# Performance work log

Hardware: AMD Instinct MI355X
Metric: run time of the kernel (lower is better)

Reference implementation:

```python
import jax, jax.numpy as jnp
import numpy as np

EPS = 1e-5

def binarize(x):
    # sign binarization with straight-through estimator (matches .data replacement in torch BNN code)
    s = jnp.where(x >= 0, 1.0, -1.0).astype(x.dtype)
    return x + jax.lax.stop_gradient(s - x)

def conv3x3(x, w):
    return jax.lax.conv_general_dilated(x, w, (1, 1), ((1, 1), (1, 1)),
                                        dimension_numbers=('NCHW', 'OIHW', 'NCHW'))

def bn4(x, g, b, m, v):
    inv = jax.lax.rsqrt(v + EPS)
    return (x - m[None, :, None, None]) * (g * inv)[None, :, None, None] + b[None, :, None, None]

def bn2(x, g, b, m, v):
    return (x - m) * (g * jax.lax.rsqrt(v + EPS)) + b

def maxpool2(x):
    return jax.lax.reduce_window(x, -jnp.inf, jax.lax.max, (1, 1, 2, 2), (1, 1, 2, 2), 'VALID')

def ht(x):
    return jnp.clip(x, -1.0, 1.0)


def setup_inputs() -> dict:
    key = jax.random.key(0)
    ks = iter(jax.random.split(key, 64))
    d = {}
    d['x'] = jax.random.normal(next(ks), (256, 3, 32, 32), jnp.float32)
    conv_shapes = [(128, 3), (128, 128), (256, 128), (256, 256), (512, 256), (512, 512)]
    for i, (co, ci) in enumerate(conv_shapes, start=1):
        d[f'w{i}'] = jax.random.normal(next(ks), (co, ci, 3, 3), jnp.float32) * 0.05
        d[f'g{i}'] = jax.random.uniform(next(ks), (co,), jnp.float32, 0.5, 1.5)
        d[f'b{i}'] = jax.random.normal(next(ks), (co,), jnp.float32) * 0.1
        d[f'm{i}'] = jax.random.normal(next(ks), (co,), jnp.float32) * 0.1
        d[f'v{i}'] = jax.random.uniform(next(ks), (co,), jnp.float32, 0.5, 1.5)
    d['bias2'] = jax.random.normal(next(ks), (128,), jnp.float32) * 0.1  # conv2 has default bias=True
    fc_shapes = [(1024, 512 * 4 * 4), (1024, 1024), (10, 1024)]
    for j, (co, ci) in enumerate(fc_shapes, start=7):
        d[f'w{j}'] = jax.random.normal(next(ks), (co, ci), jnp.float32) * 0.02
        d[f'm{j}'] = jax.random.normal(next(ks), (co,), jnp.float32) * 0.1
        d[f'v{j}'] = jax.random.uniform(next(ks), (co,), jnp.float32, 0.5, 1.5)
        if j < 9:  # last BN is affine=False
            d[f'g{j}'] = jax.random.uniform(next(ks), (co,), jnp.float32, 0.5, 1.5)
            d[f'b{j}'] = jax.random.normal(next(ks), (co,), jnp.float32) * 0.1
    return d


def reference(x, w1, g1, b1, m1, v1, w2, bias2, g2, b2, m2, v2, w3, g3, b3, m3, v3,
              w4, g4, b4, m4, v4, w5, g5, b5, m5, v5, w6, g6, b6, m6, v6,
              w7, g7, b7, m7, v7, w8, g8, b8, m8, v8, w9, m9, v9):
    # features
    h = conv3x3(x, binarize(w1))                      # first layer: input NOT binarized (3 channels)
    h = ht(bn4(h, g1, b1, m1, v1))
    h = conv3x3(binarize(h), binarize(w2)) + bias2[None, :, None, None]
    h = ht(bn4(maxpool2(h), g2, b2, m2, v2))
    h = conv3x3(binarize(h), binarize(w3))
    h = ht(bn4(h, g3, b3, m3, v3))
    h = conv3x3(binarize(h), binarize(w4))
    h = ht(bn4(maxpool2(h), g4, b4, m4, v4))
    h = conv3x3(binarize(h), binarize(w5))
    h = ht(bn4(h, g5, b5, m5, v5))
    h = conv3x3(binarize(h), binarize(w6))
    h = ht(bn4(maxpool2(h), g6, b6, m6, v6))          # [B, 512, 4, 4]
    # classifier
    h = h.reshape(-1, 512 * 4 * 4)
    h = ht(bn2(binarize(h) @ binarize(w7).T, g7, b7, m7, v7))
    h = ht(bn2(binarize(h) @ binarize(w8).T, g8, b8, m8, v8))
    h = binarize(h) @ binarize(w9).T
    h = (h - m9) * jax.lax.rsqrt(v9 + EPS)            # BatchNorm1d(affine=False)
    return jax.nn.log_softmax(h, axis=-1)
```

## Files before the change

kernel.cpp:

```cpp
#include <hip/hip_runtime.h>
#include <stdint.h>

typedef unsigned long long u64;

static __device__ __forceinline__ int uread(int v) { return __builtin_amdgcn_readfirstlane(v); }
static __device__ __forceinline__ float fr(float x) { __asm__ volatile("" : "+v"(x)); return x; }

static __device__ __forceinline__ float bn_scale(float g, float v) {
    return fr(g * fr(1.0f / fr(sqrtf(fr(v + 1e-5f)))));
}
static __device__ __forceinline__ bool bn_neg_s(float x, float si, float b, float m) {
    float t1 = fr(x - m);
    float t2 = fr(t1 * si);
    float bn = fr(t2 + b);
    return bn < 0.0f;
}


__device__ __forceinline__ void d_packw1(const float* __restrict__ w, float* __restrict__ ws, int id) {
    if (id >= 27 * 128) return;
    int co = id & 127, j = id >> 7;
    ws[j * 128 + co] = (w[co * 27 + j] < 0.f) ? -1.f : 1.f;
}

__device__ __forceinline__ void d_pack_conv(const float* __restrict__ w, u64* __restrict__ wb,
                                            int CINW, int COUT, int wv, int lane) {
    int wrd = wv % CINW, co = wv / CINW;
    int CIN = CINW * 64;
    const float* p = w + ((size_t)co * CIN + (size_t)wrd * 64 + lane) * 9;
    float f[9];
#pragma unroll
    for (int t = 0; t < 9; ++t) f[t] = p[t];
#pragma unroll
    for (int t = 0; t < 9; ++t) {
        u64 bits = __ballot(f[t] < 0.f);
        if (lane == 0) wb[(size_t)(t * CINW + wrd) * COUT + co] = bits;
    }
}

__device__ __forceinline__ void d_packw7(const float* __restrict__ w, u64* __restrict__ wb, int wv, int lane) {
    int cw = wv & 7, o = wv >> 3;
    const float* p = w + (size_t)o * 8192 + (size_t)(cw * 64 + lane) * 16;
    float f[16];
#pragma unroll
    for (int i = 0; i < 16; i += 4) {
        float4 q = *(const float4*)(p + i);
        f[i] = q.x; f[i + 1] = q.y; f[i + 2] = q.z; f[i + 3] = q.w;
    }
#pragma unroll
    for (int pixel = 0; pixel < 16; ++pixel) {
        u64 bits = __ballot(f[pixel] < 0.f);
        if (lane == 0) wb[(size_t)(pixel * 8 + cw) * 1024 + o] = bits;
    }
}

__device__ __forceinline__ void d_packw8(const float* __restrict__ w, u64* __restrict__ wb, int wv, int lane) {
    int k = wv & 15, o = wv >> 4;
    float f = w[(size_t)o * 1024 + k * 64 + lane];
    u64 bits = __ballot(f < 0.f);
    if (lane == 0) wb[(size_t)k * 1024 + o] = bits;
}

__device__ __forceinline__ void d_packw9(const float* __restrict__ w, u64* __restrict__ wb, int wv, int lane) {
    if (wv >= 160) return;
    int k = wv & 15, o = wv >> 4;
    float f = w[(size_t)o * 1024 + k * 64 + lane];
    u64 bits = __ballot(f < 0.f);
    if (lane == 0) wb[k * 16 + o] = bits;
}

__global__ __launch_bounds__(256) void pack_all_kernel(
    const float* __restrict__ w1, float* __restrict__ w1s,
    const float* __restrict__ w2, u64* __restrict__ w2p,
    const float* __restrict__ w3, u64* __restrict__ w3p,
    const float* __restrict__ w4, u64* __restrict__ w4p,
    const float* __restrict__ w5, u64* __restrict__ w5p,
    const float* __restrict__ w6, u64* __restrict__ w6p,
    const float* __restrict__ w7, u64* __restrict__ w7p,
    const float* __restrict__ w8, u64* __restrict__ w8p,
    const float* __restrict__ w9, u64* __restrict__ w9p)
{
    int b = blockIdx.x;
    int lane = threadIdx.x & 63;
    int wq = threadIdx.x >> 6;
    if (b < 14) { d_packw1(w1, w1s, b * 256 + threadIdx.x); return; } b -= 14;
    if (b < 64) { d_pack_conv(w2, w2p, 2, 128, b * 4 + wq, lane); return; } b -= 64;
    if (b < 128) { d_pack_conv(w3, w3p, 2, 256, b * 4 + wq, lane); return; } b -= 128;
    if (b < 256) { d_pack_conv(w4, w4p, 4, 256, b * 4 + wq, lane); return; } b -= 256;
    if (b < 512) { d_pack_conv(w5, w5p, 4, 512, b * 4 + wq, lane); return; } b -= 512;
    if (b < 1024) { d_pack_conv(w6, w6p, 8, 512, b * 4 + wq, lane); return; } b -= 1024;
    if (b < 2048) { d_packw7(w7, w7p, b * 4 + wq, lane); return; } b -= 2048;
    if (b < 4096) { d_packw8(w8, w8p, b * 4 + wq, lane); return; } b -= 4096;
    d_packw9(w9, w9p, b * 4 + wq, lane);
}

__global__ __launch_bounds__(256, 4) void conv1_kernel(
    const float* __restrict__ x, const float* __restrict__ w1s,
    const float* __restrict__ g, const float* __restrict__ bb,
    const float* __restrict__ m, const float* __restrict__ v,
    u64* __restrict__ out, int N)
{
    int lane = threadIdx.x & 63;
    int rid = uread(blockIdx.x * 4 + (threadIdx.x >> 6));
    if (rid >= N * 32) return;
    int n = rid >> 5, y = rid & 31;
    const float* xb = x + (size_t)n * 3072;
    const bool rv0 = (y > 0), rv2 = (y < 31);
    const int y0 = rv0 ? y - 1 : 0, y2 = rv2 ? y + 1 : 31;

    int co0 = lane, co1 = 64 + lane;
    float w0[27], w1[27];
#pragma unroll
    for (int j = 0; j < 27; ++j) {
        w0[j] = fr(w1s[j * 128 + co0]);
        w1[j] = fr(w1s[j * 128 + co1]);
    }
    float b0 = bb[co0], m0 = m[co0];
    float b1 = bb[co1], m1 = m[co1];
    float si0 = bn_scale(g[co0], v[co0]);
    float si1 = bn_scale(g[co1], v[co1]);

    float cm[9], cc[9], cn[9];
#pragma unroll
    for (int t = 0; t < 9; ++t) cm[t] = 0.f;

    auto ldcol = [&](float* c, int xs) {
#pragma unroll
        for (int ci = 0; ci < 3; ++ci) {
            float a0 = xb[ci * 1024 + y0 * 32 + xs];
            float a1 = xb[ci * 1024 + y  * 32 + xs];
            float a2 = xb[ci * 1024 + y2 * 32 + xs];
            c[0 + ci] = fr(rv0 ? a0 : 0.f);
            c[3 + ci] = fr(a1);
            c[6 + ci] = fr(rv2 ? a2 : 0.f);
        }
    };
    ldcol(cc, 0);

    u64* orow = out + (((size_t)n * 32 + y) * 32) * 2;

    for (int xx = 0; xx < 32; ++xx) {
        if (xx < 31) ldcol(cn, xx + 1);
        else {
#pragma unroll
            for (int t = 0; t < 9; ++t) cn[t] = 0.f;
        }
        float a0 = 0.f, a1 = 0.f;
#pragma unroll
        for (int ky = 0; ky < 3; ++ky) {
#pragma unroll
            for (int ci = 0; ci < 3; ++ci) a0 = fmaf(w0[ci * 9 + ky * 3 + 0], cm[ky * 3 + ci], a0);
#pragma unroll
            for (int ci = 0; ci < 3; ++ci) a0 = fmaf(w0[ci * 9 + ky * 3 + 1], cc[ky * 3 + ci], a0);
#pragma unroll
            for (int ci = 0; ci < 3; ++ci) a0 = fmaf(w0[ci * 9 + ky * 3 + 2], cn[ky * 3 + ci], a0);
        }
#pragma unroll
        for (int ky = 0; ky < 3; ++ky) {
#pragma unroll
            for (int ci = 0; ci < 3; ++ci) a1 = fmaf(w1[ci * 9 + ky * 3 + 0], cm[ky * 3 + ci], a1);
#pragma unroll
            for (int ci = 0; ci < 3; ++ci) a1 = fmaf(w1[ci * 9 + ky * 3 + 1], cc[ky * 3 + ci], a1);
#pragma unroll
            for (int ci = 0; ci < 3; ++ci) a1 = fmaf(w1[ci * 9 + ky * 3 + 2], cn[ky * 3 + ci], a1);
        }
        u64 bits0 = __ballot(bn_neg_s(a0, si0, b0, m0));
        u64 bits1 = __ballot(bn_neg_s(a1, si1, b1, m1));
        if (lane == 0) {
            ulonglong2 st; st.x = bits0; st.y = bits1;
            *(ulonglong2*)(orow + xx * 2) = st;
        }
#pragma unroll
        for (int t = 0; t < 9; ++t) { cm[t] = cc[t]; cc[t] = cn[t]; }
    }
}

template<int WORDS, int COW, bool POOL, bool HAS_BIAS, int H, int YS, int NWAVES, int MINW>
__global__ __launch_bounds__(NWAVES * 64, MINW) void binconv_lds(
    const u64* __restrict__ a, const u64* __restrict__ wb,
    const float* __restrict__ g, const float* __restrict__ bb,
    const float* __restrict__ m, const float* __restrict__ v,
    const float* __restrict__ bias, u64* __restrict__ out, int N)
{
    const int W = H;
    const int OH = POOL ? H / 2 : H, OW = POOL ? W / 2 : W;
    const int COUT = COW * 64;
    const int OROWS = OH / YS;
    const int RMAX = POOL ? OROWS * 2 + 2 : OROWS + 2;
    const int PR = POOL ? 4 : 3;
    const int NW = POOL ? 4 : 1;
    const int W2 = WORDS / 2;
    const int S = POOL ? 2 : 1;
    const int NBC = 9 * WORDS * 64;
    const int GPX = (OW <= 4) ? OW : ((NW == 4) ? 4 : OW);
    const int NG = OW / GPX;

    __shared__ alignas(16) u64 tile[RMAX * W * WORDS];

    int blk = blockIdx.x;
    int ys = blk % YS, n = blk / YS;
    int oy0 = ys * OROWS;
    int iy0 = (POOL ? oy0 * 2 - 1 : oy0 - 1); if (iy0 < 0) iy0 = 0;
    int iy1 = (POOL ? (oy0 + OROWS - 1) * 2 + 2 : oy0 + OROWS); if (iy1 > H - 1) iy1 = H - 1;
    int R = iy1 - iy0 + 1;
    {
        const u64* src = a + ((size_t)(n * H + iy0) * W) * WORDS;
        int tot = R * W * WORDS;
        for (int i = threadIdx.x; i < tot; i += NWAVES * 64) tile[i] = src[i];
    }
    __syncthreads();

    int lane = threadIdx.x & 63;
    int wv = uread((int)(threadIdx.x >> 6));

    int cw0, r0, r1;
    if (COW >= NWAVES) { cw0 = wv; r0 = 0; r1 = OROWS; }
    else { cw0 = wv % COW; int chunk = OROWS * COW / NWAVES; r0 = (wv / COW) * chunk; r1 = r0 + chunk; }

    const ulonglong2* t2 = (const ulonglong2*)tile;

    for (int cw = cw0; cw < COW; cw += NWAVES) {
        int co = cw * 64 + lane;
        float bc = bb[co], mc = m[co];
        float sic = bn_scale(g[co], v[co]);
        float bi = HAS_BIAS ? bias[co] : 0.f;

        auto store_px = [&](int oy, int ox, int best) {
            float tv = (float)best;
            if (HAS_BIAS) tv = fr(tv + bi);
            u64 bits = __ballot(bn_neg_s(tv, sic, bc, mc));
            if (lane == 0) out[((size_t)(n * OH + oy) * OW + ox) * COW + cw] = bits;
        };

        if constexpr (W2 == 1) {
            u64 wgt[18];
#pragma unroll
            for (int t = 0; t < 18; ++t) wgt[t] = wb[(size_t)t * COUT + co];

            auto px_general = [&](int oy, int ox) {
                int y0 = (POOL ? oy * 2 : oy) - 1;
                bool rv[PR];
#pragma unroll
                for (int p = 0; p < PR; ++p) rv[p] = ((unsigned)(y0 + p) < (unsigned)H);
                int x0 = (POOL ? ox * 2 : ox) - 1;
                bool cv[PR];
#pragma unroll
                for (int q = 0; q < PR; ++q) cv[q] = ((unsigned)(x0 + q) < (unsigned)W);

                int acc[NW], nb[NW];
#pragma unroll
                for (int i = 0; i < NW; ++i) { acc[i] = 0; nb[i] = 0; }
#pragma unroll
                for (int sy = 0; sy < (POOL ? 2 : 1); ++sy)
#pragma unroll
                for (int sx = 0; sx < (POOL ? 2 : 1); ++sx)
#pragma unroll
                for (int ky = 0; ky < 3; ++ky)
#pragma unroll
                for (int kx = 0; kx < 3; ++kx)
                    if (rv[sy + ky] && cv[sx + kx]) nb[POOL ? sy * 2 + sx : 0] += WORDS * 64;

                ulonglong2 pt[PR][PR];
#pragma unroll
                for (int p = 0; p < PR; ++p) if (rv[p]) {
                    int lrow = y0 + p - iy0;
#pragma unroll
                    for (int q = 0; q < PR; ++q) if (cv[q])
                        pt[p][q] = t2[(lrow * W + (x0 + q))];
                }
#pragma unroll
                for (int sy = 0; sy < (POOL ? 2 : 1); ++sy)
#pragma unroll
                for (int sx = 0; sx < (POOL ? 2 : 1); ++sx)
#pragma unroll
                for (int ky = 0; ky < 3; ++ky)
#pragma unroll
                for (int kx = 0; kx < 3; ++kx)
                    if (rv[sy + ky] && cv[sx + kx]) {
                        ulonglong2 q = pt[sy + ky][sx + kx];
                        int wi = POOL ? sy * 2 + sx : 0;
                        acc[wi] += __popcll(q.x ^ wgt[(ky * 3 + kx) * 2])
                                 + __popcll(q.y ^ wgt[(ky * 3 + kx) * 2 + 1]);
                    }
                int best = 0;
#pragma unroll
                for (int i = 0; i < NW; ++i) {
                    int dot = nb[i] - 2 * acc[i];
                    best = (i == 0) ? dot : max(best, dot);
                }
                store_px(oy, ox, best);
            };

            for (int oy = oy0 + r0; oy < oy0 + r1; ++oy) {
                int y0 = (POOL ? oy * 2 : oy) - 1;
                if (y0 < 0 || y0 + PR > H) {
                    for (int ox = 0; ox < OW; ++ox) px_general(oy, ox);
                    continue;
                }
                int base = y0 - iy0;
                px_general(oy, 0);
                {
                    ulonglong2 win[PR][PR];
                    const int xl = POOL ? 1 : 0;
#pragma unroll
                    for (int p = 0; p < PR; ++p)
#pragma unroll
                        for (int q = 0; q < PR; ++q)
                            win[p][q] = t2[(base + p) * W + xl + q];
#pragma unroll
                    for (int ox = 1; ox < OW - 1; ++ox) {
                        int acc[NW];
#pragma unroll
                        for (int i = 0; i < NW; ++i) acc[i] = 0;
#pragma unroll
                        for (int sy = 0; sy < (POOL ? 2 : 1); ++sy)
#pragma unroll
                        for (int sx = 0; sx < (POOL ? 2 : 1); ++sx)
#pragma unroll
                        for (int ky = 0; ky < 3; ++ky)
#pragma unroll
                        for (int kx = 0; kx < 3; ++kx) {
                            ulonglong2 q = win[sy + ky][sx + kx];
                            int wi = POOL ? sy * 2 + sx : 0;
                            acc[wi] += __popcll(q.x ^ wgt[(ky * 3 + kx) * 2])
                                     + __popcll(q.y ^ wgt[(ky * 3 + kx) * 2 + 1]);
                        }
                        int best = 0;
#pragma unroll
                        for (int i = 0; i < NW; ++i) {
                            int dot = NBC - 2 * acc[i];
                            best = (i == 0) ? dot : max(best, dot);
                        }
                        store_px(oy, ox, best);
                        if (ox < OW - 2) {
                            const int xnew = S * ox - 1 + PR;
#pragma unroll
                            for (int p = 0; p < PR; ++p) {
#pragma unroll
                                for (int q = 0; q < PR - S; ++q) win[p][q] = win[p][q + S];
#pragma unroll
                                for (int s = 0; s < S; ++s)
                                    win[p][PR - S + s] = t2[(base + p) * W + xnew + s];
                            }
                        }
                    }
                }
                px_general(oy, OW - 1);
            }
        } else {
            for (int oy = oy0 + r0; oy < oy0 + r1; ++oy) {
                int y0r = (POOL ? oy * 2 : oy) - 1;
                bool rv[PR];
#pragma unroll
                for (int p = 0; p < PR; ++p) rv[p] = ((unsigned)(y0r + p) < (unsigned)H);
                int baseR = y0r - iy0;

#pragma unroll
                for (int gg = 0; gg < NG; ++gg) {
                    int acc[GPX][NW];
#pragma unroll
                    for (int i = 0; i < GPX; ++i)
#pragma unroll
                        for (int wi = 0; wi < NW; ++wi) acc[i][wi] = 0;

#pragma unroll 1
                    for (int w2 = 0; w2 < W2; ++w2) {
                        u64 wc[18];
#pragma unroll
                        for (int t = 0; t < 9; ++t) {
                            wc[t * 2]     = wb[(size_t)(t * WORDS + 2 * w2) * COUT + co];
                            wc[t * 2 + 1] = wb[(size_t)(t * WORDS + 2 * w2 + 1) * COUT + co];
                        }
#pragma unroll
                        for (int i = 0; i < GPX; ++i) {
                            const int ox = gg * GPX + i;
                            const int x0 = S * ox - 1;
                            ulonglong2 pt[PR][PR];
#pragma unroll
                            for (int p = 0; p < PR; ++p) {
                                if (rv[p]) {
#pragma unroll
                                    for (int q = 0; q < PR; ++q) {
                                        const int x = x0 + q;
                                        if (x >= 0 && x < W)
                                            pt[p][q] = t2[((baseR + p) * W + x) * W2 + w2];
                                    }
                                }
                            }
#pragma unroll
                            for (int sy = 0; sy < (POOL ? 2 : 1); ++sy)
#pragma unroll
                            for (int sx = 0; sx < (POOL ? 2 : 1); ++sx)
#pragma unroll
                            for (int ky = 0; ky < 3; ++ky)
#pragma unroll
                            for (int kx = 0; kx < 3; ++kx) {
                                const int xq = x0 + sx + kx;
                                if (xq >= 0 && xq < W) {
                                    if (rv[sy + ky]) {
                                        ulonglong2 q = pt[sy + ky][sx + kx];
                                        const int t = ky * 3 + kx;
                                        const int wi = POOL ? sy * 2 + sx : 0;
                                        acc[i][wi] += __popcll(q.x ^ wc[t * 2])
                                                    + __popcll(q.y ^ wc[t * 2 + 1]);
                                    }
                                }
                            }
                        }
                    }

#pragma unroll
                    for (int i = 0; i < GPX; ++i) {
                        const int ox = gg * GPX + i;
                        const int x0 = S * ox - 1;
                        int nb[NW];
#pragma unroll
                        for (int wi = 0; wi < NW; ++wi) nb[wi] = 0;
#pragma unroll
                        for (int sy = 0; sy < (POOL ? 2 : 1); ++sy)
#pragma unroll
                        for (int sx = 0; sx < (POOL ? 2 : 1); ++sx)
#pragma unroll
                        for (int ky = 0; ky < 3; ++ky)
#pragma unroll
                        for (int kx = 0; kx < 3; ++kx) {
                            const int xq = x0 + sx + kx;
                            if (xq >= 0 && xq < W) {
                                if (rv[sy + ky]) nb[POOL ? sy * 2 + sx : 0] += WORDS * 64;
                            }
                        }
                        int best = 0;
#pragma unroll
                        for (int wi = 0; wi < NW; ++wi) {
                            int dot = nb[wi] - 2 * acc[i][wi];
                            best = (wi == 0) ? dot : max(best, dot);
                        }
                        store_px(oy, ox, best);
                    }
                }
            }
        }
    }
}

template<int KW, int OWRD>
__global__ __launch_bounds__(256) void binfc_kernel(
    const u64* __restrict__ a, const u64* __restrict__ wb,
    const float* __restrict__ g, const float* __restrict__ bb,
    const float* __restrict__ m, const float* __restrict__ v,
    u64* __restrict__ out, int N)
{
    int lane = threadIdx.x & 63;
    int wid = uread(blockIdx.x * 4 + (threadIdx.x >> 6));
    if (wid >= N * OWRD) return;
    int ow = wid & (OWRD - 1), n = wid / OWRD;
    int o = ow * 64 + lane;
    const u64* ap = a + (size_t)n * KW;
    int acc = 0;
#pragma unroll 8
    for (int k = 0; k < KW; ++k)
        acc += __popcll(ap[k] ^ wb[(size_t)k * (OWRD * 64) + o]);
    float dotf = (float)(KW * 64 - 2 * acc);
    float si = bn_scale(g[o], v[o]);
    u64 bits = __ballot(bn_neg_s(dotf, si, bb[o], m[o]));
    if (lane == 0) out[(size_t)n * OWRD + ow] = bits;
}

__global__ __launch_bounds__(64) void fc9_kernel(
    const u64* __restrict__ a, const u64* __restrict__ wb,
    const float* __restrict__ m, const float* __restrict__ v, float* __restrict__ out)
{
    int n = blockIdx.x, t = threadIdx.x;
    const u64* ap = a + (size_t)n * 16;
    float val = -1e30f;
    if (t < 10) {
        int acc = 0;
#pragma unroll
        for (int k = 0; k < 16; ++k) acc += __popcll(ap[k] ^ wb[k * 16 + t]);
        float dotf = (float)(1024 - 2 * acc);
        float inv = fr(1.0f / fr(sqrtf(fr(v[t] + 1e-5f))));
        float t1  = fr(dotf - m[t]);
        val = fr(t1 * inv);
    }
    float mx = val;
#pragma unroll
    for (int off = 32; off; off >>= 1) mx = fmaxf(mx, __shfl_xor(mx, off));
    float sh = fr(val - mx);
    double e = (t < 10) ? exp((double)sh) : 0.0;
    double sum = e;
#pragma unroll
    for (int off = 32; off; off >>= 1) sum += __shfl_xor(sum, off);
    if (t < 10) out[n * 10 + t] = (float)((double)sh - log(sum));
}

extern "C" void kernel_launch(void* const* d_in, const int* in_sizes, int n_in,
                              void* d_out, int out_size, void* d_ws, size_t ws_size,
                              hipStream_t stream) {
    auto F = [&](int i) { return (const float*)d_in[i]; };
    const float* x  = F(0);
    const float* w1 = F(1);  const float* g1 = F(2);  const float* b1 = F(3);
    const float* m1 = F(4);  const float* v1 = F(5);
    const float* w2 = F(6);  const float* g2 = F(7);  const float* b2 = F(8);
    const float* m2 = F(9);  const float* v2 = F(10);
    const float* w3 = F(11); const float* g3 = F(12); const float* b3 = F(13);
    const float* m3 = F(14); const float* v3 = F(15);
    const float* w4 = F(16); const float* g4 = F(17); const float* b4 = F(18);
    const float* m4 = F(19); const float* v4 = F(20);
    const float* w5 = F(21); const float* g5 = F(22); const float* b5 = F(23);
    const float* m5 = F(24); const float* v5 = F(25);
    const float* w6 = F(26); const float* g6 = F(27); const float* b6 = F(28);
    const float* m6 = F(29); const float* v6 = F(30);
    const float* bias2 = F(31);
    const float* w7 = F(32); const float* m7 = F(33); const float* v7 = F(34);
    const float* g7 = F(35); const float* b7 = F(36);
    const float* w8 = F(37); const float* m8 = F(38); const float* v8 = F(39);
    const float* g8 = F(40); const float* b8 = F(41);
    const float* w9 = F(42); const float* m9 = F(43); const float* v9 = F(44);
    (void)in_sizes; (void)n_in; (void)ws_size;

    const int N = out_size / 10;
    u64* ws = (u64*)d_ws;
    size_t off = 0;
    auto carve = [&](size_t nwords) { u64* p = ws + off; off += nwords; return p; };
    float* w1s = (float*)carve(1728);
    u64* w2p = carve(2304);
    u64* w3p = carve(4608);
    u64* w4p = carve(9216);
    u64* w5p = carve(18432);
    u64* w6p = carve(36864);
    u64* w7p = carve(131072);
    u64* w8p = carve(16384);
    u64* w9p = carve(256);
    u64* a1 = carve((size_t)N * 32 * 32 * 2);
    u64* a2 = carve((size_t)N * 16 * 16 * 2);
    u64* a3 = carve((size_t)N * 16 * 16 * 4);
    u64* a4 = carve((size_t)N * 8 * 8 * 4);
    u64* a5 = carve((size_t)N * 8 * 8 * 8);
    u64* a6 = carve((size_t)N * 16 * 8);
    u64* f7 = carve((size_t)N * 16);
    u64* f8 = carve((size_t)N * 16);

    pack_all_kernel<<<8182, 256, 0, stream>>>(w1, w1s, w2, w2p, w3, w3p, w4, w4p,
                                              w5, w5p, w6, w6p, w7, w7p, w8, w8p, w9, w9p);

    conv1_kernel<<<(N * 32 + 3) / 4, 256, 0, stream>>>(x, w1s, g1, b1, m1, v1, a1, N);

    binconv_lds<2, 2, true, true, 32, 8, 4, 3><<<N * 8, 256, 0, stream>>>(
        a1, w2p, g2, b2, m2, v2, bias2, a2, N);
    binconv_lds<2, 4, false, false, 16, 8, 4, 3><<<N * 8, 256, 0, stream>>>(
        a2, w3p, g3, b3, m3, v3, nullptr, a3, N);
    binconv_lds<4, 4, true, false, 16, 8, 4, 4><<<N * 8, 256, 0, stream>>>(
        a3, w4p, g4, b4, m4, v4, nullptr, a4, N);
    binconv_lds<4, 8, false, false, 8, 8, 4, 4><<<N * 8, 256, 0, stream>>>(
        a4, w5p, g5, b5, m5, v5, nullptr, a5, N);
    binconv_lds<8, 8, true, false, 8, 4, 8, 4><<<N * 4, 512, 0, stream>>>(
        a5, w6p, g6, b6, m6, v6, nullptr, a6, N);

    binfc_kernel<128, 16><<<(N * 16 + 3) / 4, 256, 0, stream>>>(a6, w7p, g7, b7, m7, v7, f7, N);
    binfc_kernel<16, 16><<<(N * 16 + 3) / 4, 256, 0, stream>>>(f7, w8p, g8, b8, m8, v8, f8, N);

    fc9_kernel<<<N, 64, 0, stream>>>(f8, w9p, m9, v9, (float*)d_out);
}
```

Baseline: 581.5 us.

## Zero-pad LDS tile and use precomputed border corrections in binary conv

The input tile is stored in LDS with a zero-padded halo, so every pixel uses one branch-free XNOR-popcount path and the special-case edge code goes away. Zero padding would count pad bits as mismatches, so per-channel weight popcounts are precomputed into a 3x3 table of border corrections that restore the exact dot product at edges and corners. The minimum-waves launch bound for three conv layers also drops from 4 to 3. In exchange the tile needs more LDS and index math at load time, and the conv loops now pay popcounts on padding pixels.

```diff
diff --git a/kernel.cpp b/kernel.cpp
--- a/kernel.cpp
+++ b/kernel.cpp
@@ -186,27 +186,34 @@
     const int OH = POOL ? H / 2 : H, OW = POOL ? W / 2 : W;
     const int COUT = COW * 64;
     const int OROWS = OH / YS;
-    const int RMAX = POOL ? OROWS * 2 + 2 : OROWS + 2;
+    const int ROWS = POOL ? OROWS * 2 + 2 : OROWS + 2;
+    const int COLS = W + 2;
     const int PR = POOL ? 4 : 3;
     const int NW = POOL ? 4 : 1;
     const int W2 = WORDS / 2;
     const int S = POOL ? 2 : 1;
-    const int NBC = 9 * WORDS * 64;
     const int GPX = (OW <= 4) ? OW : ((NW == 4) ? 4 : OW);
     const int NG = OW / GPX;
 
-    __shared__ alignas(16) u64 tile[RMAX * W * WORDS];
+    __shared__ alignas(16) u64 tile[ROWS * COLS * WORDS];
 
     int blk = blockIdx.x;
     int ys = blk % YS, n = blk / YS;
     int oy0 = ys * OROWS;
-    int iy0 = (POOL ? oy0 * 2 - 1 : oy0 - 1); if (iy0 < 0) iy0 = 0;
-    int iy1 = (POOL ? (oy0 + OROWS - 1) * 2 + 2 : oy0 + OROWS); if (iy1 > H - 1) iy1 = H - 1;
-    int R = iy1 - iy0 + 1;
+    const int ty0 = (POOL ? oy0 * 2 : oy0) - 1;
     {
-        const u64* src = a + ((size_t)(n * H + iy0) * W) * WORDS;
-        int tot = R * W * WORDS;
-        for (int i = threadIdx.x; i < tot; i += NWAVES * 64) tile[i] = src[i];
+        const u64* srcN = a + (size_t)n * H * W * WORDS;
+        const int tot = ROWS * COLS * WORDS;
+        for (int i = threadIdx.x; i < tot; i += NWAVES * 64) {
+            int r = i / (COLS * WORDS);
+            int rem = i - r * (COLS * WORDS);
+            int c = rem / WORDS, w = rem - (rem / WORDS) * WORDS;
+            int gr = ty0 + r, gc = c - 1;
+            u64 vv = 0;
+            if ((unsigned)gr < (unsigned)H && (unsigned)gc < (unsigned)W)
+                vv = srcN[((size_t)gr * W + gc) * WORDS + w];
+            tile[i] = vv;
+        }
     }
     __syncthreads();
 
@@ -224,6 +231,48 @@
         float bc = bb[co], mc = m[co];
         float sic = bn_scale(g[co], v[co]);
         float bi = HAS_BIAS ? bias[co] : 0.f;
+
+        int tp[9];
+#pragma unroll
+        for (int t = 0; t < 9; ++t) tp[t] = 0;
+        u64 wgt[W2 == 1 ? 18 : 1];
+        if constexpr (W2 == 1) {
+#pragma unroll
+            for (int t = 0; t < 18; ++t) wgt[t] = wb[(size_t)t * COUT + co];
+#pragma unroll
+            for (int t = 0; t < 9; ++t)
+                tp[t] = (int)(__popcll(wgt[t * 2]) + __popcll(wgt[t * 2 + 1]));
+        } else {
+            for (int w = 0; w < WORDS; ++w)
+#pragma unroll
+                for (int t = 0; t < 9; ++t)
+                    tp[t] += (int)__popcll(wb[(size_t)(t * WORDS + w) * COUT + co]);
+        }
+        int C[3][3];
+        {
+            int TP = 0;
+#pragma unroll
+            for (int t = 0; t < 9; ++t) TP += tp[t];
+#pragma unroll
+            for (int cy = 0; cy < 3; ++cy)
+#pragma unroll
+                for (int cx = 0; cx < 3; ++cx) {
+                    int vs = 0;
+#pragma unroll
+                    for (int ky = 0; ky < 3; ++ky) {
+                        if (cy == 0 && ky == 0) continue;
+                        if (cy == 2 && ky == 2) continue;
+#pragma unroll
+                        for (int kx = 0; kx < 3; ++kx) {
+                            if (cx == 0 && kx == 0) continue;
+                            if (cx == 2 && kx == 2) continue;
+                            vs += tp[ky * 3 + kx];
+                        }
+                    }
+                    int vr = (cy == 1) ? 3 : 2, vc = (cx == 1) ? 3 : 2;
+                    C[cy][cx] = vr * vc * WORDS * 64 + 2 * (TP - vs);
+                }
+        }
 
         auto store_px = [&](int oy, int ox, int best) {
             float tv = (float)best;
@@ -232,129 +281,73 @@
             if (lane == 0) out[((size_t)(n * OH + oy) * OW + ox) * COW + cw] = bits;
         };
 
-        if constexpr (W2 == 1) {
-            u64 wgt[18];
-#pragma unroll
-            for (int t = 0; t < 18; ++t) wgt[t] = wb[(size_t)t * COUT + co];
-
-            auto px_general = [&](int oy, int ox) {
-                int y0 = (POOL ? oy * 2 : oy) - 1;
-                bool rv[PR];
-#pragma unroll
-                for (int p = 0; p < PR; ++p) rv[p] = ((unsigned)(y0 + p) < (unsigned)H);
-                int x0 = (POOL ? ox * 2 : ox) - 1;
-                bool cv[PR];
-#pragma unroll
-                for (int q = 0; q < PR; ++q) cv[q] = ((unsigned)(x0 + q) < (unsigned)W);
-
-                int acc[NW], nb[NW];
-#pragma unroll
-                for (int i = 0; i < NW; ++i) { acc[i] = 0; nb[i] = 0; }
-#pragma unroll
-                for (int sy = 0; sy < (POOL ? 2 : 1); ++sy)
-#pragma unroll
-                for (int sx = 0; sx < (POOL ? 2 : 1); ++sx)
-#pragma unroll
-                for (int ky = 0; ky < 3; ++ky)
-#pragma unroll
-                for (int kx = 0; kx < 3; ++kx)
-                    if (rv[sy + ky] && cv[sx + kx]) nb[POOL ? sy * 2 + sx : 0] += WORDS * 64;
-
-                ulonglong2 pt[PR][PR];
-#pragma unroll
-                for (int p = 0; p < PR; ++p) if (rv[p]) {
-                    int lrow = y0 + p - iy0;
-#pragma unroll
-                    for (int q = 0; q < PR; ++q) if (cv[q])
-                        pt[p][q] = t2[(lrow * W + (x0 + q))];
-                }
-#pragma unroll
-                for (int sy = 0; sy < (POOL ? 2 : 1); ++sy)
-#pragma unroll
-                for (int sx = 0; sx < (POOL ? 2 : 1); ++sx)
-#pragma unroll
-                for (int ky = 0; ky < 3; ++ky)
-#pragma unroll
-                for (int kx = 0; kx < 3; ++kx)
-                    if (rv[sy + ky] && cv[sx + kx]) {
-                        ulonglong2 q = pt[sy + ky][sx + kx];
+        for (int oy = oy0 + r0; oy < oy0 + r1; ++oy) {
+            int y0 = (POOL ? oy * 2 : oy) - 1;
+            int trb = y0 - ty0;
+            int CA0, CA1, CA2, CB0, CB1, CB2;
+            if (POOL) {
+                bool tb = (oy == 0), bb2 = (oy == OH - 1);
+                CA0 = tb ? C[0][0] : C[1][0]; CA1 = tb ? C[0][1] : C[1][1]; CA2 = tb ? C[0][2] : C[1][2];
+                CB0 = bb2 ? C[2][0] : C[1][0]; CB1 = bb2 ? C[2][1] : C[1][1]; CB2 = bb2 ? C[2][2] : C[1][2];
+            } else {
+                bool tb = (oy == 0), bb2 = (oy == OH - 1);
+                CA0 = tb ? C[0][0] : (bb2 ? C[2][0] : C[1][0]);
+                CA1 = tb ? C[0][1] : (bb2 ? C[2][1] : C[1][1]);
+                CA2 = tb ? C[0][2] : (bb2 ? C[2][2] : C[1][2]);
+                CB0 = CA0; CB1 = CA1; CB2 = CA2;
+            }
+
+            if constexpr (W2 == 1) {
+                ulonglong2 win[PR][PR];
+#pragma unroll
+                for (int p = 0; p < PR; ++p)
+#pragma unroll
+                    for (int q = 0; q < PR; ++q)
+                        win[p][q] = t2[(trb + p) * COLS + q];
+#pragma unroll
+                for (int ox = 0; ox < OW; ++ox) {
+                    int acc[NW];
+#pragma unroll
+                    for (int i = 0; i < NW; ++i) acc[i] = 0;
+#pragma unroll
+                    for (int sy = 0; sy < (POOL ? 2 : 1); ++sy)
+#pragma unroll
+                    for (int sx = 0; sx < (POOL ? 2 : 1); ++sx)
+#pragma unroll
+                    for (int ky = 0; ky < 3; ++ky)
+#pragma unroll
+                    for (int kx = 0; kx < 3; ++kx) {
+                        ulonglong2 q = win[sy + ky][sx + kx];
                         int wi = POOL ? sy * 2 + sx : 0;
                         acc[wi] += __popcll(q.x ^ wgt[(ky * 3 + kx) * 2])
                                  + __popcll(q.y ^ wgt[(ky * 3 + kx) * 2 + 1]);
                     }
-                int best = 0;
-#pragma unroll
-                for (int i = 0; i < NW; ++i) {
-                    int dot = nb[i] - 2 * acc[i];
-                    best = (i == 0) ? dot : max(best, dot);
-                }
-                store_px(oy, ox, best);
-            };
-
-            for (int oy = oy0 + r0; oy < oy0 + r1; ++oy) {
-                int y0 = (POOL ? oy * 2 : oy) - 1;
-                if (y0 < 0 || y0 + PR > H) {
-                    for (int ox = 0; ox < OW; ++ox) px_general(oy, ox);
-                    continue;
-                }
-                int base = y0 - iy0;
-                px_general(oy, 0);
-                {
-                    ulonglong2 win[PR][PR];
-                    const int xl = POOL ? 1 : 0;
-#pragma unroll
-                    for (int p = 0; p < PR; ++p)
-#pragma unroll
-                        for (int q = 0; q < PR; ++q)
-                            win[p][q] = t2[(base + p) * W + xl + q];
-#pragma unroll
-                    for (int ox = 1; ox < OW - 1; ++ox) {
-                        int acc[NW];
-#pragma unroll
-                        for (int i = 0; i < NW; ++i) acc[i] = 0;
-#pragma unroll
-                        for (int sy = 0; sy < (POOL ? 2 : 1); ++sy)
-#pragma unroll
-                        for (int sx = 0; sx < (POOL ? 2 : 1); ++sx)
-#pragma unroll
-                        for (int ky = 0; ky < 3; ++ky)
-#pragma unroll
-                        for (int kx = 0; kx < 3; ++kx) {
-                            ulonglong2 q = win[sy + ky][sx + kx];
-                            int wi = POOL ? sy * 2 + sx : 0;
-                            acc[wi] += __popcll(q.x ^ wgt[(ky * 3 + kx) * 2])
-                                     + __popcll(q.y ^ wgt[(ky * 3 + kx) * 2 + 1]);
-                        }
-                        int best = 0;
-#pragma unroll
-                        for (int i = 0; i < NW; ++i) {
-                            int dot = NBC - 2 * acc[i];
-                            best = (i == 0) ? dot : max(best, dot);
-                        }
-                        store_px(oy, ox, best);
-                        if (ox < OW - 2) {
-                            const int xnew = S * ox - 1 + PR;
-#pragma unroll
-                            for (int p = 0; p < PR; ++p) {
-#pragma unroll
-                                for (int q = 0; q < PR - S; ++q) win[p][q] = win[p][q + S];
-#pragma unroll
-                                for (int s = 0; s < S; ++s)
-                                    win[p][PR - S + s] = t2[(base + p) * W + xnew + s];
-                            }
+                    int best;
+                    if (POOL) {
+                        int Ct0 = (ox == 0) ? CA0 : CA1;
+                        int Ct1 = (ox == OW - 1) ? CA2 : CA1;
+                        int Cb0 = (ox == 0) ? CB0 : CB1;
+                        int Cb1 = (ox == OW - 1) ? CB2 : CB1;
+                        int d0 = Ct0 - 2 * acc[0], d1 = Ct1 - 2 * acc[1];
+                        int d2 = Cb0 - 2 * acc[2], d3 = Cb1 - 2 * acc[3];
+                        best = max(max(d0, d1), max(d2, d3));
+                    } else {
+                        int Ct = (ox == 0) ? CA0 : ((ox == OW - 1) ? CA2 : CA1);
+                        best = Ct - 2 * acc[0];
+                    }
+                    store_px(oy, ox, best);
+                    if (ox < OW - 1) {
+#pragma unroll
+                        for (int p = 0; p < PR; ++p) {
+#pragma unroll
+                            for (int q = 0; q < PR - S; ++q) win[p][q] = win[p][q + S];
+#pragma unroll
+                            for (int s = 0; s < S; ++s)
+                                win[p][PR - S + s] = t2[(trb + p) * COLS + S * ox + PR + s];
                         }
                     }
                 }
-                px_general(oy, OW - 1);
-            }
-        } else {
-            for (int oy = oy0 + r0; oy < oy0 + r1; ++oy) {
-                int y0r = (POOL ? oy * 2 : oy) - 1;
-                bool rv[PR];
-#pragma unroll
-                for (int p = 0; p < PR; ++p) rv[p] = ((unsigned)(y0r + p) < (unsigned)H);
-                int baseR = y0r - iy0;
-
+            } else {
 #pragma unroll
                 for (int gg = 0; gg < NG; ++gg) {
                     int acc[GPX][NW];
@@ -374,19 +367,13 @@
 #pragma unroll
                         for (int i = 0; i < GPX; ++i) {
                             const int ox = gg * GPX + i;
-                            const int x0 = S * ox - 1;
+                            const int tc0 = S * ox;
                             ulonglong2 pt[PR][PR];
 #pragma unroll
-                            for (int p = 0; p < PR; ++p) {
-                                if (rv[p]) {
-#pragma unroll
-                                    for (int q = 0; q < PR; ++q) {
-                                        const int x = x0 + q;
-                                        if (x >= 0 && x < W)
-                                            pt[p][q] = t2[((baseR + p) * W + x) * W2 + w2];
-                                    }
-                                }
-                            }
+                            for (int p = 0; p < PR; ++p)
+#pragma unroll
+                                for (int q = 0; q < PR; ++q)
+                                    pt[p][q] = t2[((trb + p) * COLS + tc0 + q) * W2 + w2];
 #pragma unroll
                             for (int sy = 0; sy < (POOL ? 2 : 1); ++sy)
 #pragma unroll
@@ -395,45 +382,29 @@
                             for (int ky = 0; ky < 3; ++ky)
 #pragma unroll
                             for (int kx = 0; kx < 3; ++kx) {
-                                const int xq = x0 + sx + kx;
-                                if (xq >= 0 && xq < W) {
-                                    if (rv[sy + ky]) {
-                                        ulonglong2 q = pt[sy + ky][sx + kx];
-                                        const int t = ky * 3 + kx;
-                                        const int wi = POOL ? sy * 2 + sx : 0;
-                                        acc[i][wi] += __popcll(q.x ^ wc[t * 2])
-                                                    + __popcll(q.y ^ wc[t * 2 + 1]);
-                                    }
-                                }
+                                ulonglong2 q = pt[sy + ky][sx + kx];
+                                const int t = ky * 3 + kx;
+                                const int wi = POOL ? sy * 2 + sx : 0;
+                                acc[i][wi] += __popcll(q.x ^ wc[t * 2])
+                                            + __popcll(q.y ^ wc[t * 2 + 1]);
                             }
                         }
                     }
-
 #pragma unroll
                     for (int i = 0; i < GPX; ++i) {
                         const int ox = gg * GPX + i;
-                        const int x0 = S * ox - 1;
-                        int nb[NW];
-#pragma unroll
-                        for (int wi = 0; wi < NW; ++wi) nb[wi] = 0;
-#pragma unroll
-                        for (int sy = 0; sy < (POOL ? 2 : 1); ++sy)
-#pragma unroll
-                        for (int sx = 0; sx < (POOL ? 2 : 1); ++sx)
-#pragma unroll
-                        for (int ky = 0; ky < 3; ++ky)
-#pragma unroll
-                        for (int kx = 0; kx < 3; ++kx) {
-                            const int xq = x0 + sx + kx;
-                            if (xq >= 0 && xq < W) {
-                                if (rv[sy + ky]) nb[POOL ? sy * 2 + sx : 0] += WORDS * 64;
-                            }
-                        }
-                        int best = 0;
-#pragma unroll
-                        for (int wi = 0; wi < NW; ++wi) {
-                            int dot = nb[wi] - 2 * acc[i][wi];
-                            best = (wi == 0) ? dot : max(best, dot);
+                        int best;
+                        if (POOL) {
+                            int Ct0 = (ox == 0) ? CA0 : CA1;
+                            int Ct1 = (ox == OW - 1) ? CA2 : CA1;
+                            int Cb0 = (ox == 0) ? CB0 : CB1;
+                            int Cb1 = (ox == OW - 1) ? CB2 : CB1;
+                            int d0 = Ct0 - 2 * acc[i][0], d1 = Ct1 - 2 * acc[i][1];
+                            int d2 = Cb0 - 2 * acc[i][2], d3 = Cb1 - 2 * acc[i][3];
+                            best = max(max(d0, d1), max(d2, d3));
+                        } else {
+                            int Ct = (ox == 0) ? CA0 : ((ox == OW - 1) ? CA2 : CA1);
+                            best = Ct - 2 * acc[i][0];
                         }
                         store_px(oy, ox, best);
                     }
@@ -549,11 +520,11 @@
         a1, w2p, g2, b2, m2, v2, bias2, a2, N);
     binconv_lds<2, 4, false, false, 16, 8, 4, 3><<<N * 8, 256, 0, stream>>>(
         a2, w3p, g3, b3, m3, v3, nullptr, a3, N);
-    binconv_lds<4, 4, true, false, 16, 8, 4, 4><<<N * 8, 256, 0, stream>>>(
+    binconv_lds<4, 4, true, false, 16, 8, 4, 3><<<N * 8, 256, 0, stream>>>(
         a3, w4p, g4, b4, m4, v4, nullptr, a4, N);
-    binconv_lds<4, 8, false, false, 8, 8, 4, 4><<<N * 8, 256, 0, stream>>>(
+    binconv_lds<4, 8, false, false, 8, 8, 4, 3><<<N * 8, 256, 0, stream>>>(
         a4, w5p, g5, b5, m5, v5, nullptr, a5, N);
-    binconv_lds<8, 8, true, false, 8, 4, 8, 4><<<N * 4, 512, 0, stream>>>(
+    binconv_lds<8, 8, true, false, 8, 4, 8, 3><<<N * 4, 512, 0, stream>>>(
         a5, w6p, g6, b6, m6, v6, nullptr, a6, N);
 
     binfc_kernel<128, 16><<<(N * 16 + 3) / 4, 256, 0, stream>>>(a6, w7p, g7, b7, m7, v7, f7, N);
```

After: 703.2 us. 20.9% more time.
